# Performance work log

Measured on AMD Instinct MI355X. Metric: run time of the kernel, lower is better.

The kernel has to match this reference:

```python
import jax, jax.numpy as jnp
import numpy as np

B, L, D, H = 2, 2048, 2048, 16
C = D // H  # head dim = 128
EPS = 1e-5


def setup_inputs() -> dict:
    key = jax.random.key(0)
    k1, k2, k3, k4 = jax.random.split(key, 4)
    scale = 1.0 / np.sqrt(D)
    return {
        "x": jax.random.normal(k1, (B, L, D), dtype=jnp.float32),
        "theta": jax.random.uniform(k2, (B, L, D // 2), dtype=jnp.float32) * 6.2831853,
        "w_qkv": jax.random.normal(k3, (3 * D, D), dtype=jnp.float32) * scale,
        "w_y": jax.random.normal(k4, (D, D), dtype=jnp.float32) * scale,
        "b_y": jnp.zeros((D,), dtype=jnp.float32),
    }


def _rms_norm(t):
    # RMSNorm over last dim, eps=1e-5, no affine
    return t * jax.lax.rsqrt(jnp.mean(t * t, axis=-1, keepdims=True) + EPS)


def _apply_rope(q, k, theta):
    # q, k: (B, H, L, C); theta: (B, H, L, C//2)
    qr, qi = q[..., 0::2], q[..., 1::2]
    kr, ki = k[..., 0::2], k[..., 1::2]
    cos_t, sin_t = jnp.cos(theta), jnp.sin(theta)
    q_rot = jnp.stack((qr * cos_t - qi * sin_t, qr * sin_t + qi * cos_t), axis=-1).reshape(q.shape)
    k_rot = jnp.stack((kr * cos_t - ki * sin_t, kr * sin_t + ki * cos_t), axis=-1).reshape(k.shape)
    return q_rot, k_rot


def reference(x, theta, w_qkv, w_y, b_y):
    # QKV projection: (B, L, 3D)
    qkv = jnp.einsum("bld,ed->ble", x, w_qkv)
    # rearrange '... L (n H C) -> n ... H L C'
    qkv = qkv.reshape(B, L, 3, H, C).transpose(2, 0, 3, 1, 4)  # (3, B, H, L, C)
    q, k, v = qkv[0], qkv[1], qkv[2]
    q, k = _rms_norm(q), _rms_norm(k)
    # theta: (B, L, H*C/2) -> (B, H, L, C/2)
    th = theta.reshape(B, L, H, C // 2).transpose(0, 2, 1, 3)
    q, k = _apply_rope(q, k, th)
    # scaled dot-product attention
    scores = jnp.einsum("bhqc,bhkc->bhqk", q, k) / np.sqrt(C).astype(np.float32)
    attn = jax.nn.softmax(scores, axis=-1)
    y = jnp.einsum("bhqk,bhkc->bhqc", attn, v)
    # (B, H, L, C) -> (B, L, H*C)
    y = y.transpose(0, 2, 1, 3).reshape(B, L, D)
    return jnp.einsum("bld,ed->ble", y, w_y) + b_y
```

## Files before the change

### kernel.cpp

```cpp
#include <hip/hip_runtime.h>
#include <stdint.h>

typedef uint16_t u16;
typedef __attribute__((ext_vector_type(8))) short bf16x8;
typedef __attribute__((ext_vector_type(4))) float f32x4;


__device__ __forceinline__ u16 f2bf(float f) {
  uint32_t u = __builtin_bit_cast(uint32_t, f);
  u += 0x7fffu + ((u >> 16) & 1u);
  return (u16)(u >> 16);
}
__device__ __forceinline__ float bf2f(u16 h) {
  return __builtin_bit_cast(float, (uint32_t)h << 16);
}
__device__ __forceinline__ uint32_t pack2bf(float a, float b) {
  uint32_t ua = __builtin_bit_cast(uint32_t, a) + 0x7fffu;
  uint32_t ub = __builtin_bit_cast(uint32_t, b) + 0x7fffu;
  return (ua >> 16) | (ub & 0xffff0000u);
}
__device__ __forceinline__ void gl_lds16(const u16* g, u16* l) {
  __builtin_amdgcn_global_load_lds((const __attribute__((address_space(1))) uint32_t*)g,
                                   (__attribute__((address_space(3))) uint32_t*)l, 16, 0, 0);
}

__global__ __launch_bounds__(256) void castk(const float* __restrict__ in,
                                             u16* __restrict__ out, int n) {
  int idx = (blockIdx.x * 256 + threadIdx.x) * 4;
  int stride = gridDim.x * 256 * 4;
  for (int i = idx; i < n; i += stride) {
    float4 v = *(const float4*)(in + i);
    uint32_t lo = (uint32_t)f2bf(v.x) | ((uint32_t)f2bf(v.y) << 16);
    uint32_t hi = (uint32_t)f2bf(v.z) | ((uint32_t)f2bf(v.w) << 16);
    *(uint2*)(out + i) = make_uint2(lo, hi);
  }
}

__global__ __launch_bounds__(512, 2) void gemm8_qkv(
    const u16* __restrict__ A, const u16* __restrict__ Bw,
    u16* __restrict__ qb, u16* __restrict__ kb, u16* __restrict__ vt) {
  __shared__ u16 sm[57344];
  const int K = 2048;
  const int tid = threadIdx.x, lane = tid & 63;
  const int wid = tid >> 6, g = lane >> 4, lr = lane & 15;
  const int wm = wid >> 2, wn = wid & 3;
  const int m0 = blockIdx.y * 256, n0 = blockIdx.x * 192;
  const int x7 = lr & 7;
  const int srow = tid >> 3, sj = tid & 7, sjs = sj ^ (srow & 7);

  auto stA = [&](int buf, int kt, int R) {
    gl_lds16(A + (size_t)(m0 + R + srow) * K + kt * 64 + sjs * 8,
             &sm[buf * 28672 + R * 64 + tid * 8]);
  };
  auto stB = [&](int buf, int kt, int R) {
    gl_lds16(Bw + (size_t)(n0 + R + srow) * K + kt * 64 + sjs * 8,
             &sm[buf * 28672 + 16384 + R * 64 + tid * 8]);
  };

  f32x4 acc[8][3] = {};

  stB(0, 0, 0); stB(0, 0, 64); stB(0, 0, 128);
  stA(0, 0, 0); stA(0, 0, 128);
  stA(0, 0, 64); stA(0, 0, 192);
  asm volatile("s_waitcnt vmcnt(2)" ::: "memory");
  __builtin_amdgcn_s_barrier();

  for (int t = 0; t < 32; ++t) {
    const int cur = t & 1, nxt = cur ^ 1;
    const int kn = (t < 31) ? t + 1 : 31;
    const u16* As = &sm[cur * 28672];
    const u16* Bs = &sm[cur * 28672 + 16384];
    bf16x8 bfr[3][2];
#pragma unroll
    for (int p = 0; p < 4; ++p) {
      bf16x8 af[2][2];
#pragma unroll
      for (int i = 0; i < 2; ++i)
#pragma unroll
        for (int ks = 0; ks < 2; ++ks)
          af[i][ks] = *(const bf16x8*)&As[(wm * 128 + (p * 2 + i) * 16 + lr) * 64 +
                                          (((ks * 4 + g) ^ x7) * 8)];
      if (p == 0) {
#pragma unroll
        for (int nf = 0; nf < 3; ++nf) {
          int rb = wn * 48 + nf * 16 + lr;
#pragma unroll
          for (int ks = 0; ks < 2; ++ks)
            bfr[nf][ks] = *(const bf16x8*)&Bs[rb * 64 + (((ks * 4 + g) ^ (rb & 7)) * 8)];
        }
        stB(nxt, kn, 0);
        stB(nxt, kn, 64);
        stB(nxt, kn, 128);
      } else if (p == 1) {
        stA(nxt, kn, 0);
        stA(nxt, kn, 128);
      } else if (p == 2) {
        stA(nxt, kn, 64);
        stA(nxt, kn, 192);
      }
      __builtin_amdgcn_s_barrier();
      asm volatile("s_waitcnt lgkmcnt(0)" ::: "memory");
      __builtin_amdgcn_sched_barrier(0);
      __builtin_amdgcn_s_setprio(1);
#pragma unroll
      for (int i = 0; i < 2; ++i)
#pragma unroll
        for (int nf = 0; nf < 3; ++nf) {
          acc[p * 2 + i][nf] = __builtin_amdgcn_mfma_f32_16x16x32_bf16(
              af[i][0], bfr[nf][0], acc[p * 2 + i][nf], 0, 0, 0);
          acc[p * 2 + i][nf] = __builtin_amdgcn_mfma_f32_16x16x32_bf16(
              af[i][1], bfr[nf][1], acc[p * 2 + i][nf], 0, 0, 0);
        }
      __builtin_amdgcn_s_setprio(0);
      if (p == 1) asm volatile("s_waitcnt vmcnt(5)" ::: "memory");
      if (p == 3) asm volatile("s_waitcnt vmcnt(2)" ::: "memory");
      __builtin_amdgcn_s_barrier();
    }
  }
  asm volatile("s_waitcnt vmcnt(0)" ::: "memory");

#pragma unroll
  for (int mf = 0; mf < 8; ++mf)
#pragma unroll
    for (int nf = 0; nf < 3; ++nf) {
      int n = n0 + wn * 48 + nf * 16 + lr;
      int s = n >> 11, h = (n >> 7) & 15, cb = n & 127;
#pragma unroll
      for (int r = 0; r < 4; ++r) {
        int m = m0 + wm * 128 + mf * 16 + g * 4 + r;
        int b = m >> 11, lp = m & 2047;
        u16 val = f2bf(acc[mf][nf][r]);
        if (s == 0)
          qb[(size_t)((b * 16 + h) * 2048 + lp) * 128 + cb] = val;
        else if (s == 1)
          kb[(size_t)((b * 16 + h) * 2048 + lp) * 128 + cb] = val;
        else
          vt[(size_t)((b * 16 + h) * 128 + cb) * 2048 + lp] = val;
      }
    }
}

__global__ __launch_bounds__(256) void gemm_out(
    const u16* __restrict__ A, const u16* __restrict__ Bw, int K,
    float* __restrict__ out, const float* __restrict__ bias) {
  __shared__ u16 As[128 * 64];
  __shared__ u16 Bs[128 * 64];
  const int tid = threadIdx.x;
  const int lane = tid & 63, wid = tid >> 6;
  const int g = lane >> 4, lr = lane & 15;
  const int wm = wid >> 1, wn = wid & 1;
  const int m0 = blockIdx.y * 128, n0 = blockIdx.x * 128;
  f32x4 acc[4][4] = {};
  const int nk = K >> 6;
  for (int kt = 0; kt < nk; ++kt) {
    const int kbase = kt * 64;
#pragma unroll
    for (int i = 0; i < 4; ++i) {
      int ci = wid * 256 + i * 64 + lane;
      int row = ci >> 3, j = ci & 7;
      int js = j ^ (row & 7);
      gl_lds16(A + (size_t)(m0 + row) * K + kbase + js * 8, &As[(wid * 256 + i * 64) * 8]);
    }
#pragma unroll
    for (int i = 0; i < 4; ++i) {
      int ci = wid * 256 + i * 64 + lane;
      int row = ci >> 3, j = ci & 7;
      int js = j ^ (row & 7);
      gl_lds16(Bw + (size_t)(n0 + row) * K + kbase + js * 8, &Bs[(wid * 256 + i * 64) * 8]);
    }
    __syncthreads();
#pragma unroll
    for (int ks = 0; ks < 2; ++ks) {
      bf16x8 af[4], bfr[4];
#pragma unroll
      for (int t = 0; t < 4; ++t) {
        int ra = wm * 64 + t * 16 + lr;
        af[t] = *(const bf16x8*)&As[ra * 64 + (((ks * 4 + g) ^ (ra & 7)) * 8)];
        int rb = wn * 64 + t * 16 + lr;
        bfr[t] = *(const bf16x8*)&Bs[rb * 64 + (((ks * 4 + g) ^ (rb & 7)) * 8)];
      }
#pragma unroll
      for (int mt = 0; mt < 4; ++mt)
#pragma unroll
        for (int nt = 0; nt < 4; ++nt)
          acc[mt][nt] =
              __builtin_amdgcn_mfma_f32_16x16x32_bf16(af[mt], bfr[nt], acc[mt][nt], 0, 0, 0);
    }
    __syncthreads();
  }
#pragma unroll
  for (int mt = 0; mt < 4; ++mt)
#pragma unroll
    for (int nt = 0; nt < 4; ++nt) {
      int n = n0 + wn * 64 + nt * 16 + lr;
      float bv = bias[n];
#pragma unroll
      for (int r = 0; r < 4; ++r) {
        int m = m0 + wm * 64 + mt * 16 + g * 4 + r;
        out[(size_t)m * 2048 + n] = acc[mt][nt][r] + bv;
      }
    }
}

__global__ __launch_bounds__(256) void qk_fix(u16* __restrict__ qb, u16* __restrict__ kb,
                                              const float* __restrict__ theta) {
  const int row = blockIdx.x * 4 + (threadIdx.x >> 6);
  const int lane = threadIdx.x & 63;
  const int bh = row >> 11, l = row & 2047;
  const int b = bh >> 4, h = bh & 15;
  float th = theta[(size_t)(b * 2048 + l) * 1024 + h * 64 + lane];
  float sn, cs;
  __sincosf(th, &sn, &cs);
#pragma unroll
  for (int which = 0; which < 2; ++which) {
    u16* buf = which ? kb : qb;
    uint32_t* p = (uint32_t*)(buf + (size_t)row * 128) + lane;
    uint32_t v = *p;
    float x0 = bf2f((u16)(v & 0xffff)), x1 = bf2f((u16)(v >> 16));
    float ss = x0 * x0 + x1 * x1;
#pragma unroll
    for (int m = 1; m <= 32; m <<= 1) ss += __shfl_xor(ss, m);
    float rn = rsqrtf(ss * (1.0f / 128.0f) + 1e-5f);
    if (which == 0) rn *= 0.12751743f;
    x0 *= rn;
    x1 *= rn;
    float y0 = x0 * cs - x1 * sn;
    float y1 = x0 * sn + x1 * cs;
    *p = (uint32_t)f2bf(y0) | ((uint32_t)f2bf(y1) << 16);
  }
}

__global__ __launch_bounds__(256, 2) void attn_k(const u16* __restrict__ qb,
                                                 const u16* __restrict__ kb,
                                                 const u16* __restrict__ vt,
                                                 u16* __restrict__ yb) {
  __shared__ u16 sm[32768];
  const int gid = blockIdx.x;
  const int slot = gid & 7, rest = gid >> 3;
  const int bh = slot * 4 + (rest & 3);
  const int qtile = rest >> 2;
  const int b = bh >> 4, h = bh & 15;
  const int tid = threadIdx.x, lane = tid & 63, wid = tid >> 6;
  const int g = lane >> 4, lr = lane & 15;
  const int q0 = qtile * 128 + wid * 32;

  bf16x8 qf[2][4];
#pragma unroll
  for (int qs = 0; qs < 2; ++qs) {
    const u16* qrow = qb + (size_t)(bh * 2048 + q0 + qs * 16 + lr) * 128;
#pragma unroll
    for (int ks = 0; ks < 4; ++ks) qf[qs][ks] = *(const bf16x8*)&qrow[ks * 32 + g * 8];
  }

  auto stage = [&](int buf, int kv) {
#pragma unroll
    for (int i = 0; i < 4; ++i) {
      int ci = i * 256 + tid;
      int row = ci >> 4, j = ci & 15;
      gl_lds16(kb + (size_t)(bh * 2048 + kv + row) * 128 + (j ^ (row & 7)) * 8,
               &sm[buf * 8192 + ci * 8]);
    }
#pragma unroll
    for (int i = 0; i < 4; ++i) {
      int ci = i * 256 + tid;
      int row = ci >> 3, j = ci & 7;
      gl_lds16(vt + (size_t)(bh * 128 + row) * 2048 + kv + (j ^ (row & 7)) * 8,
               &sm[16384 + buf * 8192 + ci * 8]);
    }
  };

  f32x4 acc[2][8] = {};
  float mrun[2] = {-1e30f, -1e30f}, lrun[2] = {0.f, 0.f};
  const int sA = (2 * (g & 1)) * 16 + lr, sB = sA + 16;
  const bool hi2 = (g >> 1) != 0;

  stage(0, 0);
  asm volatile("s_waitcnt vmcnt(0)" ::: "memory");
  __builtin_amdgcn_s_barrier();

  for (int t = 0; t < 32; ++t) {
    const int cur = t & 1;
    if (t < 31) stage(cur ^ 1, (t + 1) * 64);
    const u16* Ks = &sm[cur * 8192];
    const u16* Vs = &sm[16384 + cur * 8192];

    f32x4 st[2][4] = {};
#pragma unroll
    for (int ks = 0; ks < 4; ++ks) {
      bf16x8 kf[4];
#pragma unroll
      for (int kt = 0; kt < 4; ++kt) {
        int row = kt * 16 + lr;
        kf[kt] = *(const bf16x8*)&Ks[row * 128 + (((ks * 4 + g) ^ (row & 7)) * 8)];
      }
#pragma unroll
      for (int kt = 0; kt < 4; ++kt)
#pragma unroll
        for (int qs = 0; qs < 2; ++qs)
          st[qs][kt] =
              __builtin_amdgcn_mfma_f32_16x16x32_bf16(kf[kt], qf[qs][ks], st[qs][kt], 0, 0, 0);
    }

    float pmax[2];
#pragma unroll
    for (int qs = 0; qs < 2; ++qs) {
      float mx = st[qs][0][0];
#pragma unroll
      for (int kt = 0; kt < 4; ++kt)
#pragma unroll
        for (int r = 0; r < 4; ++r) mx = fmaxf(mx, st[qs][kt][r]);
      mx = fmaxf(mx, __shfl_xor(mx, 16));
      mx = fmaxf(mx, __shfl_xor(mx, 32));
      pmax[qs] = mx;
    }
    float need = fmaxf(pmax[0] - mrun[0], pmax[1] - mrun[1]);
    if (!__all(need <= 8.0f)) {
#pragma unroll
      for (int qs = 0; qs < 2; ++qs) {
        float mnew = fmaxf(mrun[qs], pmax[qs]);
        float corr = __builtin_amdgcn_exp2f(mrun[qs] - mnew);
        lrun[qs] *= corr;
        mrun[qs] = mnew;
#pragma unroll
        for (int ct = 0; ct < 8; ++ct) {
          acc[qs][ct][0] *= corr;
          acc[qs][ct][1] *= corr;
          acc[qs][ct][2] *= corr;
          acc[qs][ct][3] *= corr;
        }
      }
    }
    uint32_t pw[2][4][2];
#pragma unroll
    for (int qs = 0; qs < 2; ++qs) {
      float rsum = 0.f;
#pragma unroll
      for (int kt = 0; kt < 4; ++kt)
#pragma unroll
        for (int hf = 0; hf < 2; ++hf) {
          float e0 = __builtin_amdgcn_exp2f(st[qs][kt][2 * hf] - mrun[qs]);
          float e1 = __builtin_amdgcn_exp2f(st[qs][kt][2 * hf + 1] - mrun[qs]);
          rsum += e0 + e1;
          pw[qs][kt][hf] = pack2bf(e0, e1);
        }
      rsum += __shfl_xor(rsum, 16);
      rsum += __shfl_xor(rsum, 32);
      lrun[qs] += rsum;
    }

#pragma unroll
    for (int ks2 = 0; ks2 < 2; ++ks2) {
      bf16x8 pf[2];
#pragma unroll
      for (int qs = 0; qs < 2; ++qs) {
        uint32_t a0 = __shfl(pw[qs][ks2 * 2][0], sA);
        uint32_t a1 = __shfl(pw[qs][ks2 * 2][1], sA);
        uint32_t a2 = __shfl(pw[qs][ks2 * 2][0], sB);
        uint32_t a3 = __shfl(pw[qs][ks2 * 2][1], sB);
        uint32_t b0 = __shfl(pw[qs][ks2 * 2 + 1][0], sA);
        uint32_t b1 = __shfl(pw[qs][ks2 * 2 + 1][1], sA);
        uint32_t b2 = __shfl(pw[qs][ks2 * 2 + 1][0], sB);
        uint32_t b3 = __shfl(pw[qs][ks2 * 2 + 1][1], sB);
        union {
          uint32_t u[4];
          bf16x8 v;
        } tt;
        tt.u[0] = hi2 ? b0 : a0;
        tt.u[1] = hi2 ? b1 : a1;
        tt.u[2] = hi2 ? b2 : a2;
        tt.u[3] = hi2 ? b3 : a3;
        pf[qs] = tt.v;
      }
#pragma unroll
      for (int ct = 0; ct < 8; ++ct) {
        int row = ct * 16 + lr;
        bf16x8 vf = *(const bf16x8*)&Vs[row * 64 + (((ks2 * 4 + g) ^ (row & 7)) * 8)];
#pragma unroll
        for (int qs = 0; qs < 2; ++qs)
          acc[qs][ct] = __builtin_amdgcn_mfma_f32_16x16x32_bf16(vf, pf[qs], acc[qs][ct], 0, 0, 0);
      }
    }
    if (t < 31) {
      asm volatile("s_waitcnt vmcnt(0)" ::: "memory");
      __builtin_amdgcn_s_barrier();
    }
  }

#pragma unroll
  for (int qs = 0; qs < 2; ++qs) {
    float inv = 1.f / lrun[qs];
    const size_t orow = (size_t)(b * 2048 + q0 + qs * 16 + lr) * 2048 + h * 128;
#pragma unroll
    for (int ct = 0; ct < 8; ++ct) {
      uint32_t lo = pack2bf(acc[qs][ct][0] * inv, acc[qs][ct][1] * inv);
      uint32_t hi = pack2bf(acc[qs][ct][2] * inv, acc[qs][ct][3] * inv);
      *(uint2*)&yb[orow + ct * 16 + g * 4] = make_uint2(lo, hi);
    }
  }
}

extern "C" void kernel_launch(void* const* d_in, const int* in_sizes, int n_in,
                              void* d_out, int out_size, void* d_ws, size_t ws_size,
                              hipStream_t stream) {
  const float* x = (const float*)d_in[0];
  const float* theta = (const float*)d_in[1];
  const float* wqkv = (const float*)d_in[2];
  const float* wy = (const float*)d_in[3];
  const float* by = (const float*)d_in[4];
  float* out = (float*)d_out;
  char* ws = (char*)d_ws;
  u16* xb  = (u16*)(ws + 0);
  u16* wqb = (u16*)(ws + 16777216);
  u16* wyb = (u16*)(ws + 41943040);
  u16* qb  = (u16*)(ws + 50331648);
  u16* kb  = (u16*)(ws + 67108864);
  u16* vt  = (u16*)(ws + 83886080);
  u16* yb  = (u16*)(ws + 100663296);

  castk<<<2048, 256, 0, stream>>>(x, xb, 2 * 2048 * 2048);
  castk<<<2048, 256, 0, stream>>>(wqkv, wqb, 3 * 2048 * 2048);
  castk<<<1024, 256, 0, stream>>>(wy, wyb, 2048 * 2048);

  gemm8_qkv<<<dim3(32, 16), 512, 0, stream>>>(xb, wqb, qb, kb, vt);
  qk_fix<<<16384, 256, 0, stream>>>(qb, kb, theta);
  attn_k<<<512, 256, 0, stream>>>(qb, kb, vt, yb);
  gemm_out<<<dim3(16, 32), 256, 0, stream>>>(yb, wyb, 2048, out, by);
}
```

Measured before the change: 305.1 us.

## Software-pipeline LDS fragment reads in QKV GEMM and drop per-phase barrier

The QKV GEMM main loop now double-buffers its register fragments: A fragments for the next phase, and B fragments for the next k-tile, are read from LDS before the current MFMAs are issued. This is meant to hide LDS read latency behind matrix math, and it removes the trailing barrier and the explicit lgkmcnt wait in each phase. Launch bounds drop to one block per SM so the extra fragment registers fit, at the cost of occupancy. The attention K staging is split into two half-loops with recomputed indices, which appears to produce the same addresses and is mostly a code reshuffle.

```diff
diff --git a/kernel.cpp b/kernel.cpp
--- a/kernel.cpp
+++ b/kernel.cpp
@@ -36,7 +36,7 @@
   }
 }
 
-__global__ __launch_bounds__(512, 2) void gemm8_qkv(
+__global__ __launch_bounds__(512, 1) void gemm8_qkv(
     const u16* __restrict__ A, const u16* __restrict__ Bw,
     u16* __restrict__ qb, u16* __restrict__ kb, u16* __restrict__ vt) {
   __shared__ u16 sm[57344];
@@ -45,8 +45,7 @@
   const int wid = tid >> 6, g = lane >> 4, lr = lane & 15;
   const int wm = wid >> 2, wn = wid & 3;
   const int m0 = blockIdx.y * 256, n0 = blockIdx.x * 192;
-  const int x7 = lr & 7;
-  const int srow = tid >> 3, sj = tid & 7, sjs = sj ^ (srow & 7);
+  const int srow = tid >> 3, sjs = (tid & 7) ^ (srow & 7);
 
   auto stA = [&](int buf, int kt, int R) {
     gl_lds16(A + (size_t)(m0 + R + srow) * K + kt * 64 + sjs * 8,
@@ -56,66 +55,91 @@
     gl_lds16(Bw + (size_t)(n0 + R + srow) * K + kt * 64 + sjs * 8,
              &sm[buf * 28672 + 16384 + R * 64 + tid * 8]);
   };
+  auto rdA = [&](const u16* As, int mf, int ks) {
+    int ra = wm * 128 + mf * 16 + lr;
+    return *(const bf16x8*)&As[ra * 64 + (((ks * 4 + g) ^ (ra & 7)) * 8)];
+  };
+  auto rdB = [&](const u16* Bs, int nf, int ks) {
+    int rb = wn * 48 + nf * 16 + lr;
+    return *(const bf16x8*)&Bs[rb * 64 + (((ks * 4 + g) ^ (rb & 7)) * 8)];
+  };
 
   f32x4 acc[8][3] = {};
+  bf16x8 bc[3][2], bn[3][2], afc[2][2], afn[2][2];
 
   stB(0, 0, 0); stB(0, 0, 64); stB(0, 0, 128);
   stA(0, 0, 0); stA(0, 0, 128);
   stA(0, 0, 64); stA(0, 0, 192);
   asm volatile("s_waitcnt vmcnt(2)" ::: "memory");
   __builtin_amdgcn_s_barrier();
+  {
+    const u16* As0 = &sm[0];
+    const u16* Bs0 = &sm[16384];
+#pragma unroll
+    for (int nf = 0; nf < 3; ++nf)
+#pragma unroll
+      for (int ks = 0; ks < 2; ++ks) bc[nf][ks] = rdB(Bs0, nf, ks);
+#pragma unroll
+    for (int i = 0; i < 2; ++i)
+#pragma unroll
+      for (int ks = 0; ks < 2; ++ks) afn[i][ks] = rdA(As0, i, ks);
+  }
 
   for (int t = 0; t < 32; ++t) {
     const int cur = t & 1, nxt = cur ^ 1;
     const int kn = (t < 31) ? t + 1 : 31;
-    const u16* As = &sm[cur * 28672];
-    const u16* Bs = &sm[cur * 28672 + 16384];
-    bf16x8 bfr[3][2];
+    const u16* Asc = &sm[cur * 28672];
+    const u16* Asn = &sm[nxt * 28672];
+    const u16* Bsn = &sm[nxt * 28672 + 16384];
+
 #pragma unroll
     for (int p = 0; p < 4; ++p) {
-      bf16x8 af[2][2];
 #pragma unroll
       for (int i = 0; i < 2; ++i)
 #pragma unroll
-        for (int ks = 0; ks < 2; ++ks)
-          af[i][ks] = *(const bf16x8*)&As[(wm * 128 + (p * 2 + i) * 16 + lr) * 64 +
-                                          (((ks * 4 + g) ^ x7) * 8)];
+        for (int ks = 0; ks < 2; ++ks) afc[i][ks] = afn[i][ks];
       if (p == 0) {
-#pragma unroll
-        for (int nf = 0; nf < 3; ++nf) {
-          int rb = wn * 48 + nf * 16 + lr;
-#pragma unroll
-          for (int ks = 0; ks < 2; ++ks)
-            bfr[nf][ks] = *(const bf16x8*)&Bs[rb * 64 + (((ks * 4 + g) ^ (rb & 7)) * 8)];
-        }
-        stB(nxt, kn, 0);
-        stB(nxt, kn, 64);
-        stB(nxt, kn, 128);
+        stB(nxt, kn, 0); stB(nxt, kn, 64); stB(nxt, kn, 128);
+        asm volatile("s_waitcnt vmcnt(3)" ::: "memory");
       } else if (p == 1) {
-        stA(nxt, kn, 0);
-        stA(nxt, kn, 128);
+        stA(nxt, kn, 0); stA(nxt, kn, 128);
       } else if (p == 2) {
-        stA(nxt, kn, 64);
-        stA(nxt, kn, 192);
+        stA(nxt, kn, 64); stA(nxt, kn, 192);
+      } else {
+        asm volatile("s_waitcnt vmcnt(2)" ::: "memory");
       }
       __builtin_amdgcn_s_barrier();
-      asm volatile("s_waitcnt lgkmcnt(0)" ::: "memory");
-      __builtin_amdgcn_sched_barrier(0);
+      if (p < 3) {
+#pragma unroll
+        for (int i = 0; i < 2; ++i)
+#pragma unroll
+          for (int ks = 0; ks < 2; ++ks) afn[i][ks] = rdA(Asc, (p + 1) * 2 + i, ks);
+      } else {
+#pragma unroll
+        for (int nf = 0; nf < 3; ++nf)
+#pragma unroll
+          for (int ks = 0; ks < 2; ++ks) bn[nf][ks] = rdB(Bsn, nf, ks);
+#pragma unroll
+        for (int i = 0; i < 2; ++i)
+#pragma unroll
+          for (int ks = 0; ks < 2; ++ks) afn[i][ks] = rdA(Asn, i, ks);
+      }
       __builtin_amdgcn_s_setprio(1);
 #pragma unroll
       for (int i = 0; i < 2; ++i)
 #pragma unroll
         for (int nf = 0; nf < 3; ++nf) {
           acc[p * 2 + i][nf] = __builtin_amdgcn_mfma_f32_16x16x32_bf16(
-              af[i][0], bfr[nf][0], acc[p * 2 + i][nf], 0, 0, 0);
+              afc[i][0], bc[nf][0], acc[p * 2 + i][nf], 0, 0, 0);
           acc[p * 2 + i][nf] = __builtin_amdgcn_mfma_f32_16x16x32_bf16(
-              af[i][1], bfr[nf][1], acc[p * 2 + i][nf], 0, 0, 0);
+              afc[i][1], bc[nf][1], acc[p * 2 + i][nf], 0, 0, 0);
         }
       __builtin_amdgcn_s_setprio(0);
-      if (p == 1) asm volatile("s_waitcnt vmcnt(5)" ::: "memory");
-      if (p == 3) asm volatile("s_waitcnt vmcnt(2)" ::: "memory");
-      __builtin_amdgcn_s_barrier();
-    }
+    }
+#pragma unroll
+    for (int nf = 0; nf < 3; ++nf)
+#pragma unroll
+      for (int ks = 0; ks < 2; ++ks) bc[nf][ks] = bn[nf][ks];
   }
   asm volatile("s_waitcnt vmcnt(0)" ::: "memory");
 
@@ -254,11 +278,18 @@
 
   auto stage = [&](int buf, int kv) {
 #pragma unroll
-    for (int i = 0; i < 4; ++i) {
+    for (int i = 0; i < 2; ++i) {
       int ci = i * 256 + tid;
       int row = ci >> 4, j = ci & 15;
       gl_lds16(kb + (size_t)(bh * 2048 + kv + row) * 128 + (j ^ (row & 7)) * 8,
                &sm[buf * 8192 + ci * 8]);
+    }
+#pragma unroll
+    for (int i = 2; i < 4; ++i) {
+      int ci = (i - 2) * 256 + tid;
+      int row = ci >> 4, j = ci & 15;
+      gl_lds16(kb + (size_t)(bh * 2048 + kv + 32 + row) * 128 + (j ^ (row & 7)) * 8,
+               &sm[buf * 8192 + 4096 + ci * 8]);
     }
 #pragma unroll
     for (int i = 0; i < 4; ++i) {
```

Result: no change. 303.2 us (-0.6%).
